# Kernel optimization log

Hardware: AMD Instinct MI355X
Metric: run time of the kernel (lower is better)

The kernel has to match this reference:

```python
import jax, jax.numpy as jnp
import numpy as np

N = 50000       # nodes
E = 800000      # edges (before self-loops)
F_IN = 128
HID = 64
HEADS = 4
OUT_DIM = 128
N_CLS = 2
NG = 500        # num graphs
SLOPE = 0.2     # GATConv leaky_relu negative slope
EPS = 1e-5      # BatchNorm eps


def setup_inputs() -> dict:
    key = jax.random.key(0)
    ks = jax.random.split(key, 24)
    s = 0.05
    d = {
        "x": jax.random.normal(ks[0], (N, F_IN), jnp.float32),
        "edge_index": jax.random.randint(ks[1], (2, E), 0, N, jnp.int64),
        "batch": jnp.sort(jax.random.randint(ks[2], (N,), 0, NG, jnp.int64)),
        # GATConv 1
        "W1": jax.random.normal(ks[3], (F_IN, HEADS * HID), jnp.float32) * s,
        "att_src1": jax.random.normal(ks[4], (HEADS, HID), jnp.float32) * s,
        "att_dst1": jax.random.normal(ks[5], (HEADS, HID), jnp.float32) * s,
        "b1": jnp.zeros((HEADS * HID,), jnp.float32),
        # BN1 (eval mode)
        "g1": jnp.ones((HEADS * HID,), jnp.float32),
        "be1": jnp.zeros((HEADS * HID,), jnp.float32),
        "rm1": jnp.zeros((HEADS * HID,), jnp.float32),
        "rv1": jnp.ones((HEADS * HID,), jnp.float32),
        # GATConv 2
        "W2": jax.random.normal(ks[6], (HEADS * HID, HEADS * HID), jnp.float32) * s,
        "att_src2": jax.random.normal(ks[7], (HEADS, HID), jnp.float32) * s,
        "att_dst2": jax.random.normal(ks[8], (HEADS, HID), jnp.float32) * s,
        "b2": jnp.zeros((HEADS * HID,), jnp.float32),
        # BN2 (eval mode)
        "g2": jnp.ones((HEADS * HID,), jnp.float32),
        "be2": jnp.zeros((HEADS * HID,), jnp.float32),
        "rm2": jnp.zeros((HEADS * HID,), jnp.float32),
        "rv2": jnp.ones((HEADS * HID,), jnp.float32),
        # MLP head
        "lw1": jax.random.normal(ks[9], (HEADS * HID, OUT_DIM), jnp.float32) * s,
        "lb1": jnp.zeros((OUT_DIM,), jnp.float32),
        "lw2": jax.random.normal(ks[10], (OUT_DIM, N_CLS), jnp.float32) * s,
        "lb2": jnp.zeros((N_CLS,), jnp.float32),
    }
    return d


def _gat_conv(x, src, dst, W, a_src, a_dst, b):
    """PyG GATConv (concat heads, add_self_loops=True, eval -> no dropout)."""
    n = x.shape[0]
    h = (x @ W).reshape(n, HEADS, -1)            # [N, H, C]
    loop = jnp.arange(n)
    s = jnp.concatenate([src, loop])             # self-loops appended
    d = jnp.concatenate([dst, loop])
    a_s = jnp.sum(h * a_src, axis=-1)            # [N, H]
    a_d = jnp.sum(h * a_dst, axis=-1)            # [N, H]
    e = jax.nn.leaky_relu(a_s[s] + a_d[d], SLOPE)   # [Et, H]
    # softmax over incoming edges per destination node
    m = jax.ops.segment_max(e, d, num_segments=n)
    ex = jnp.exp(e - m[d])
    denom = jax.ops.segment_sum(ex, d, num_segments=n)
    alpha = ex / denom[d]                        # [Et, H]
    msg = h[s] * alpha[:, :, None]               # [Et, H, C]
    out = jax.ops.segment_sum(msg, d, num_segments=n)
    return out.reshape(n, -1) + b


def _bn_eval(x, g, be, rm, rv):
    return (x - rm) * jax.lax.rsqrt(rv + EPS) * g + be


def reference(x, edge_index, batch, W1, att_src1, att_dst1, b1, g1, be1, rm1, rv1,
              W2, att_src2, att_dst2, b2, g2, be2, rm2, rv2, lw1, lb1, lw2, lb2):
    src, dst = edge_index[0], edge_index[1]
    h = jax.nn.relu(_gat_conv(x, src, dst, W1, att_src1, att_dst1, b1))
    h = _bn_eval(h, g1, be1, rm1, rv1)
    h = jax.nn.relu(_gat_conv(h, src, dst, W2, att_src2, att_dst2, b2))
    h = _bn_eval(h, g2, be2, rm2, rv2)
    # global mean pool over graphs
    sums = jax.ops.segment_sum(h, batch, num_segments=NG)
    cnt = jax.ops.segment_sum(jnp.ones((h.shape[0],), h.dtype), batch, num_segments=NG)
    pooled = sums / jnp.clip(cnt, 1.0)[:, None]
    z = jax.nn.relu(pooled @ lw1 + lb1)
    return z @ lw2 + lb2
```

## Files before the change

### kernel.cpp

```cpp
#include <hip/hip_runtime.h>
#include <hip/hip_bf16.h>
#include <math.h>

#define N_NODES 50000
#define M_PAD   50048
#define TILE_M  64
#define NBLK_GEMM (M_PAD / TILE_M)
#define N_EDGES 800000
#define F_IN 128
#define HID 64
#define HEADS 4
#define FEAT 256
#define OUT_DIM 128
#define N_CLS 2
#define NG 500
#define SLOPE 0.2f
#define BN_EPS 1e-5f
#define ECAP 64
#define ET (N_EDGES + N_NODES)
#define EH ((ET + 1) / 2)
#define NBLK_BUILD ((EH + 255) / 256)

typedef __attribute__((ext_vector_type(8))) short short8;
typedef __attribute__((ext_vector_type(4))) float floatx4;
typedef __attribute__((ext_vector_type(2))) float floatx2;

__device__ inline unsigned short f2bf(float f) {
    unsigned int u = __float_as_uint(f);
    unsigned int lsb = (u >> 16) & 1u;
    return (unsigned short)((u + 0x7fffu + lsb) >> 16);
}

template<bool AF32, bool BUILD>
__global__ __launch_bounds__(256, 4) void gemm_mfma_gat(
    const void* __restrict__ Av, const unsigned short* __restrict__ BT,
    const float* __restrict__ att_src, const float* __restrict__ att_dst,
    unsigned char* __restrict__ h8, float* __restrict__ a_s,
    float* __restrict__ a_d, int K,
    const int* __restrict__ src, const int* __restrict__ dst,
    int* __restrict__ deg, int* __restrict__ ell,
    int* __restrict__ ovf_cnt, int* __restrict__ ovf) {
    constexpr int LS = 40;
    constexpr int C8 = 272;
    __shared__ __align__(16) unsigned char smem_raw[(TILE_M + FEAT) * LS * 2];
    int t = threadIdx.x;

    if (BUILD && blockIdx.x >= NBLK_GEMM) {
        int i = (blockIdx.x - NBLK_GEMM) * 256 + t;
        if (i >= EH) return;
        int ss[2], dd[2], pp[2];
        int nv = 0;
        #pragma unroll
        for (int j = 0; j < 2; j++) {
            int e = i + j * EH;
            if (e < ET) {
                if (e < N_EDGES) { ss[nv] = src[e]; dd[nv] = dst[e]; }
                else             { ss[nv] = dd[nv] = e - N_EDGES; }
                nv++;
            }
        }
        #pragma unroll
        for (int j = 0; j < 2; j++)
            if (j < nv) pp[j] = atomicAdd(&deg[dd[j]], 1);
        #pragma unroll
        for (int j = 0; j < 2; j++) {
            if (j >= nv) continue;
            if (pp[j] < ECAP) {
                ell[dd[j] * ECAP + pp[j]] = ss[j];
            } else {
                int k = atomicAdd(ovf_cnt, 1);
                ovf[2 * k] = ss[j];
                ovf[2 * k + 1] = dd[j];
            }
        }
        return;
    }

    unsigned short* As = (unsigned short*)smem_raw;
    unsigned short* Bs = As + TILE_M * LS;
    unsigned char*  s8 = smem_raw;
    int lane = t & 63, w = t >> 6;
    int row0 = blockIdx.x * TILE_M;
    int mrow = lane & 15, quad = lane >> 4;

    floatx4 acc[4][4] = {};

    int rA = t >> 2, cA = (t & 3) * 8;

    const unsigned short* Ab = (const unsigned short*)Av;
    const float* Af = (const float*)Av;

    for (int k0 = 0; k0 < K; k0 += 32) {
        {
            int r = rA;
            if (AF32) {
                uint4 pk = make_uint4(0, 0, 0, 0);
                if (row0 + r < N_NODES) {
                    float4 f0 = *(const float4*)&Af[(long long)(row0 + r) * K + k0 + cA];
                    float4 f1 = *(const float4*)&Af[(long long)(row0 + r) * K + k0 + cA + 4];
                    pk.x = (unsigned)f2bf(f0.x) | ((unsigned)f2bf(f0.y) << 16);
                    pk.y = (unsigned)f2bf(f0.z) | ((unsigned)f2bf(f0.w) << 16);
                    pk.z = (unsigned)f2bf(f1.x) | ((unsigned)f2bf(f1.y) << 16);
                    pk.w = (unsigned)f2bf(f1.z) | ((unsigned)f2bf(f1.w) << 16);
                }
                *(uint4*)&As[r * LS + cA] = pk;
            } else {
                *(uint4*)&As[r * LS + cA] = *(const uint4*)&Ab[(long long)(row0 + r) * K + k0 + cA];
            }
        }
        #pragma unroll
        for (int j = 0; j < 4; j++) {
            int r = rA + j * 64;
            *(uint4*)&Bs[r * LS + cA] = *(const uint4*)&BT[(long long)r * K + k0 + cA];
        }
        __syncthreads();
        short8 bf[4];
        #pragma unroll
        for (int ni = 0; ni < 4; ni++)
            bf[ni] = *(const short8*)&Bs[(w * 64 + ni * 16 + mrow) * LS + quad * 8];
        #pragma unroll
        for (int mi = 0; mi < 4; mi++) {
            short8 af = *(const short8*)&As[(mi * 16 + mrow) * LS + quad * 8];
            #pragma unroll
            for (int ni = 0; ni < 4; ni++)
                acc[mi][ni] = __builtin_amdgcn_mfma_f32_16x16x32_bf16(af, bf[ni],
                                                                      acc[mi][ni], 0, 0, 0);
        }
        __syncthreads();
    }

    float ats[4], atd[4];
    #pragma unroll
    for (int ni = 0; ni < 4; ni++) {
        ats[ni] = att_src[w * 64 + ni * 16 + mrow];
        atd[ni] = att_dst[w * 64 + ni * 16 + mrow];
    }
    #pragma unroll
    for (int mi = 0; mi < 4; mi++) {
        #pragma unroll
        for (int r = 0; r < 4; r++) {
            int row = row0 + mi * 16 + quad * 4 + r;
            float ps = 0.f, pd = 0.f;
            #pragma unroll
            for (int ni = 0; ni < 4; ni++) {
                float v = acc[mi][ni][r];
                ps += v * ats[ni];
                pd += v * atd[ni];
            }
            #pragma unroll
            for (int off = 1; off < 16; off <<= 1) {
                ps += __shfl_xor(ps, off);
                pd += __shfl_xor(pd, off);
            }
            if (mrow == 0 && row < N_NODES) {
                a_s[row * 4 + w] = ps;
                a_d[row * 4 + w] = pd;
            }
        }
    }

    #pragma unroll
    for (int mi = 0; mi < 4; mi++)
        #pragma unroll
        for (int r = 0; r < 4; r++) {
            int row = mi * 16 + quad * 4 + r;
            #pragma unroll
            for (int ni = 0; ni < 4; ni += 2) {
                int pk = __builtin_amdgcn_cvt_pk_fp8_f32(acc[mi][ni][r],
                                                         acc[mi][ni + 1][r], 0, false);
                s8[row * C8 + w * 64 + ni * 16 + mrow]       = (unsigned char)(pk & 0xff);
                s8[row * C8 + w * 64 + (ni + 1) * 16 + mrow] = (unsigned char)((pk >> 8) & 0xff);
            }
        }
    __syncthreads();
    {
        int r2 = t >> 2, q = t & 3;
        const uint4* sp = (const uint4*)&s8[r2 * C8 + q * 64];
        uint4* dp = (uint4*)&h8[(long long)(row0 + r2) * FEAT + q * 64];
        #pragma unroll
        for (int k = 0; k < 4; k++)
            dp[k] = sp[k];
    }
}

__global__ void prep(const float* __restrict__ W1, const float* __restrict__ W2,
                     unsigned short* __restrict__ W1T, unsigned short* __restrict__ W2T,
                     int* __restrict__ deg, int* __restrict__ ovf_cnt,
                     unsigned long long* __restrict__ h1bf_pad) {
    int i = blockIdx.x * 256 + threadIdx.x;
    if (i < F_IN * 256) {
        int k = i >> 8, n = i & 255;
        W1T[n * F_IN + k] = f2bf(W1[i]);
    }
    int j = i - F_IN * 256;
    if (j >= 0 && j < FEAT * 256) {
        int k = j >> 8, n = j & 255;
        W2T[n * FEAT + k] = f2bf(W2[j]);
    }
    if (i < N_NODES) deg[i] = 0;
    if (i == 0) *ovf_cnt = 0;
    if (i < (M_PAD - N_NODES) * FEAT / 4) h1bf_pad[i] = 0ULL;
}

__global__ __launch_bounds__(256) void gat_fused(
    const int* __restrict__ deg_arr, const int* __restrict__ ell,
    const int* __restrict__ ovf_cnt, const int* __restrict__ ovf,
    const float* __restrict__ a_s, const float* __restrict__ a_d,
    const unsigned char* __restrict__ h8, const float* __restrict__ bias,
    const float* __restrict__ g, const float* __restrict__ be,
    const float* __restrict__ rm, const float* __restrict__ rv,
    unsigned short* __restrict__ out16) {
    int t = threadIdx.x;
    int lane = t & 63;
    int w = t >> 6;
    int hd = lane >> 4;
    int d = blockIdx.x * 4 + w;

    __shared__ float p_lds[4 * ECAP * 4];
    __shared__ int   o_lds[4 * ECAP];
    float* pw = &p_lds[w * ECAP * 4];
    int*   ow = &o_lds[w * ECAP];

    const unsigned int* __restrict__ H1 = (const unsigned int*)h8;

    int deg = deg_arr[d];
    float4 ad4 = *(const float4*)&a_d[d * 4];

    float den = 0.f;
    float4 acc = make_float4(0.f, 0.f, 0.f, 0.f);

    if (deg <= ECAP) {
        float lg[4] = {-INFINITY, -INFINITY, -INFINITY, -INFINITY};
        if (lane < deg) {
            int s = ell[d * ECAP + lane];
            ow[lane] = s * 64;
            float4 as4 = *(const float4*)&a_s[s * 4];
            float e0 = as4.x + ad4.x; lg[0] = e0 > 0.f ? e0 : SLOPE * e0;
            float e1 = as4.y + ad4.y; lg[1] = e1 > 0.f ? e1 : SLOPE * e1;
            float e2 = as4.z + ad4.z; lg[2] = e2 > 0.f ? e2 : SLOPE * e2;
            float e3 = as4.w + ad4.w; lg[3] = e3 > 0.f ? e3 : SLOPE * e3;
        }
        float mm = fmaxf(fmaxf(lg[0], lg[1]), fmaxf(lg[2], lg[3]));
        #pragma unroll
        for (int off = 1; off < 64; off <<= 1) mm = fmaxf(mm, __shfl_xor(mm, off));
        if (lane < deg) {
            float4 pq;
            pq.x = __expf(lg[0] - mm);
            pq.y = __expf(lg[1] - mm);
            pq.z = __expf(lg[2] - mm);
            pq.w = __expf(lg[3] - mm);
            *(float4*)&pw[lane * 4] = pq;
        }
        int e = 0;
        for (; e + 1 < deg; e += 2) {
            int oA = ow[e], oB = ow[e + 1];
            float pA = pw[e * 4 + hd], pB = pw[(e + 1) * 4 + hd];
            int uA = (int)H1[oA + lane];
            int uB = (int)H1[oB + lane];
            den += pA + pB;
            floatx2 a0 = __builtin_amdgcn_cvt_pk_f32_fp8(uA, false);
            floatx2 a1 = __builtin_amdgcn_cvt_pk_f32_fp8(uA, true);
            floatx2 b0 = __builtin_amdgcn_cvt_pk_f32_fp8(uB, false);
            floatx2 b1 = __builtin_amdgcn_cvt_pk_f32_fp8(uB, true);
            acc.x += pA * a0.x; acc.y += pA * a0.y;
            acc.z += pA * a1.x; acc.w += pA * a1.y;
            acc.x += pB * b0.x; acc.y += pB * b0.y;
            acc.z += pB * b1.x; acc.w += pB * b1.y;
        }
        if (e < deg) {
            int oA = ow[e];
            float pA = pw[e * 4 + hd];
            int uA = (int)H1[oA + lane];
            den += pA;
            floatx2 a0 = __builtin_amdgcn_cvt_pk_f32_fp8(uA, false);
            floatx2 a1 = __builtin_amdgcn_cvt_pk_f32_fp8(uA, true);
            acc.x += pA * a0.x; acc.y += pA * a0.y;
            acc.z += pA * a1.x; acc.w += pA * a1.y;
        }
    } else {
        float m_old;
        {
            int s = ell[d * ECAP + lane];
            ow[lane] = s * 64;
            float4 as4 = *(const float4*)&a_s[s * 4];
            float lg[4];
            float e0 = as4.x + ad4.x; lg[0] = e0 > 0.f ? e0 : SLOPE * e0;
            float e1 = as4.y + ad4.y; lg[1] = e1 > 0.f ? e1 : SLOPE * e1;
            float e2 = as4.z + ad4.z; lg[2] = e2 > 0.f ? e2 : SLOPE * e2;
            float e3 = as4.w + ad4.w; lg[3] = e3 > 0.f ? e3 : SLOPE * e3;
            float mm = fmaxf(fmaxf(lg[0], lg[1]), fmaxf(lg[2], lg[3]));
            #pragma unroll
            for (int off = 1; off < 64; off <<= 1) mm = fmaxf(mm, __shfl_xor(mm, off));
            m_old = mm;
            float4 pq;
            pq.x = __expf(lg[0] - mm);
            pq.y = __expf(lg[1] - mm);
            pq.z = __expf(lg[2] - mm);
            pq.w = __expf(lg[3] - mm);
            *(float4*)&pw[lane * 4] = pq;
            for (int e = 0; e < ECAP; e++) {
                int oA = ow[e];
                float pA = pw[e * 4 + hd];
                int uA = (int)H1[oA + lane];
                den += pA;
                floatx2 a0 = __builtin_amdgcn_cvt_pk_f32_fp8(uA, false);
                floatx2 a1 = __builtin_amdgcn_cvt_pk_f32_fp8(uA, true);
                acc.x += pA * a0.x; acc.y += pA * a0.y;
                acc.z += pA * a1.x; acc.w += pA * a1.y;
            }
        }
        int nov = *ovf_cnt;
        for (int i = 0; i < nov; i++) {
            int s2 = ovf[2 * i], d2 = ovf[2 * i + 1];
            if (d2 != d) continue;
            float4 as4 = *(const float4*)&a_s[s2 * 4];
            float lg[4];
            float e0 = as4.x + ad4.x; lg[0] = e0 > 0.f ? e0 : SLOPE * e0;
            float e1 = as4.y + ad4.y; lg[1] = e1 > 0.f ? e1 : SLOPE * e1;
            float e2 = as4.z + ad4.z; lg[2] = e2 > 0.f ? e2 : SLOPE * e2;
            float e3 = as4.w + ad4.w; lg[3] = e3 > 0.f ? e3 : SLOPE * e3;
            float mmax = fmaxf(fmaxf(lg[0], lg[1]), fmaxf(lg[2], lg[3]));
            float m_new = fmaxf(m_old, mmax);
            float alpha = __expf(m_old - m_new);
            m_old = m_new;
            float ph = __expf(lg[hd] - m_new);
            acc.x *= alpha; acc.y *= alpha; acc.z *= alpha; acc.w *= alpha;
            den = den * alpha + ph;
            int u = (int)H1[s2 * 64 + lane];
            floatx2 a0 = __builtin_amdgcn_cvt_pk_f32_fp8(u, false);
            floatx2 a1 = __builtin_amdgcn_cvt_pk_f32_fp8(u, true);
            acc.x += ph * a0.x; acc.y += ph * a0.y;
            acc.z += ph * a1.x; acc.w += ph * a1.y;
        }
    }
    float inv = 1.f / den;
    int c0 = lane * 4;
    float4 bi = *(const float4*)&bias[c0];
    float4 gg = *(const float4*)&g[c0];
    float4 bb = *(const float4*)&be[c0];
    float4 mm4 = *(const float4*)&rm[c0];
    float4 vv = *(const float4*)&rv[c0];
    float v0 = fmaxf(acc.x * inv + bi.x, 0.f);
    float v1 = fmaxf(acc.y * inv + bi.y, 0.f);
    float v2 = fmaxf(acc.z * inv + bi.z, 0.f);
    float v3 = fmaxf(acc.w * inv + bi.w, 0.f);
    v0 = (v0 - mm4.x) * rsqrtf(vv.x + BN_EPS) * gg.x + bb.x;
    v1 = (v1 - mm4.y) * rsqrtf(vv.y + BN_EPS) * gg.y + bb.y;
    v2 = (v2 - mm4.z) * rsqrtf(vv.z + BN_EPS) * gg.z + bb.z;
    v3 = (v3 - mm4.w) * rsqrtf(vv.w + BN_EPS) * gg.w + bb.w;
    unsigned long long o =
        (unsigned long long)f2bf(v0) |
        ((unsigned long long)f2bf(v1) << 16) |
        ((unsigned long long)f2bf(v2) << 32) |
        ((unsigned long long)f2bf(v3) << 48);
    __builtin_nontemporal_store(o, (unsigned long long*)&out16[(long long)d * FEAT + c0]);
}

__global__ __launch_bounds__(256) void head_fused(
    const unsigned short* __restrict__ h2, const int* __restrict__ batch,
    const float* __restrict__ lw1, const float* __restrict__ lb1,
    const float* __restrict__ lw2, const float* __restrict__ lb2,
    float* __restrict__ out) {
    int gph = blockIdx.x;
    int t = threadIdx.x;
    __shared__ float pooled[FEAT];
    __shared__ float zl[OUT_DIM];
    __shared__ int lo_s, hi_s;
    if (t == 0) {
        int lo = 0, hi = N_NODES;
        while (lo < hi) { int mid = (lo + hi) >> 1; if (batch[mid] < gph) lo = mid + 1; else hi = mid; }
        lo_s = lo;
        int lo2 = 0, hi2 = N_NODES;
        while (lo2 < hi2) { int mid = (lo2 + hi2) >> 1; if (batch[mid] < gph + 1) lo2 = mid + 1; else hi2 = mid; }
        hi_s = lo2;
    }
    __syncthreads();
    int lo = lo_s, hi = hi_s;
    float a0 = 0.f, a1 = 0.f, a2 = 0.f, a3 = 0.f;
    int n = lo;
    for (; n + 3 < hi; n += 4) {
        a0 += __uint_as_float((unsigned)h2[(long long)n * FEAT + t] << 16);
        a1 += __uint_as_float((unsigned)h2[(long long)(n + 1) * FEAT + t] << 16);
        a2 += __uint_as_float((unsigned)h2[(long long)(n + 2) * FEAT + t] << 16);
        a3 += __uint_as_float((unsigned)h2[(long long)(n + 3) * FEAT + t] << 16);
    }
    for (; n < hi; n++) a0 += __uint_as_float((unsigned)h2[(long long)n * FEAT + t] << 16);
    float cnt = fmaxf((float)(hi - lo), 1.f);
    pooled[t] = (a0 + a1 + a2 + a3) / cnt;
    __syncthreads();
    int j = t >> 1, kh = t & 1;
    float zp = 0.f;
    #pragma unroll 8
    for (int k = kh * 128; k < kh * 128 + 128; k++)
        zp += pooled[k] * lw1[k * OUT_DIM + j];
    zp += __shfl_xor(zp, 1);
    if (kh == 0) zl[j] = fmaxf(zp + lb1[j], 0.f);
    __syncthreads();
    int w = t >> 6, lane = t & 63;
    if (w < 2) {
        float p = zl[lane] * lw2[lane * 2 + w] + zl[lane + 64] * lw2[(lane + 64) * 2 + w];
        #pragma unroll
        for (int off = 1; off < 64; off <<= 1) p += __shfl_xor(p, off);
        if (lane == 0) out[gph * 2 + w] = p + lb2[w];
    }
}

extern "C" void kernel_launch(void* const* d_in, const int* in_sizes, int n_in,
                              void* d_out, int out_size, void* d_ws, size_t ws_size,
                              hipStream_t stream) {
    const float* x       = (const float*)d_in[0];
    const int*   ei      = (const int*)d_in[1];
    const int*   batch   = (const int*)d_in[2];
    const float* W1      = (const float*)d_in[3];
    const float* att_s1  = (const float*)d_in[4];
    const float* att_d1  = (const float*)d_in[5];
    const float* b1      = (const float*)d_in[6];
    const float* g1      = (const float*)d_in[7];
    const float* be1     = (const float*)d_in[8];
    const float* rm1     = (const float*)d_in[9];
    const float* rv1     = (const float*)d_in[10];
    const float* W2      = (const float*)d_in[11];
    const float* att_s2  = (const float*)d_in[12];
    const float* att_d2  = (const float*)d_in[13];
    const float* b2      = (const float*)d_in[14];
    const float* g2      = (const float*)d_in[15];
    const float* be2     = (const float*)d_in[16];
    const float* rm2     = (const float*)d_in[17];
    const float* rv2     = (const float*)d_in[18];
    const float* lw1     = (const float*)d_in[19];
    const float* lb1     = (const float*)d_in[20];
    const float* lw2     = (const float*)d_in[21];
    const float* lb2     = (const float*)d_in[22];
    float* out           = (float*)d_out;

    const int* src = ei;
    const int* dst = ei + N_EDGES;

    char* p = (char*)d_ws;
    auto carve = [&p](size_t bytes) -> void* {
        void* r = (void*)p;
        p += (bytes + 63) & ~(size_t)63;
        return r;
    };
    unsigned short* h2bf = (unsigned short*)carve(sizeof(short) * (size_t)N_NODES * FEAT);
    float* a_s    = (float*)carve(sizeof(float) * N_NODES * HEADS);
    float* a_d    = (float*)carve(sizeof(float) * N_NODES * HEADS);
    int*   deg    = (int*)carve(sizeof(int) * N_NODES);
    int*   ell    = (int*)carve(sizeof(int) * (size_t)N_NODES * ECAP);
    int*   ovf_cnt= (int*)carve(sizeof(int) * 16);
    int*   ovf    = (int*)carve(sizeof(int) * 2 * ET);
    unsigned char*  h8   = (unsigned char*)carve((size_t)M_PAD * FEAT);
    unsigned short* h1bf = (unsigned short*)carve(sizeof(short) * (size_t)M_PAD * FEAT);
    unsigned short* w1t  = (unsigned short*)carve(sizeof(short) * FEAT * F_IN);
    unsigned short* w2t  = (unsigned short*)carve(sizeof(short) * FEAT * FEAT);

    prep<<<((F_IN + FEAT) * 256 + 255) / 256, 256, 0, stream>>>(
        W1, W2, w1t, w2t, deg, ovf_cnt,
        (unsigned long long*)(h1bf + (size_t)N_NODES * FEAT));

    gemm_mfma_gat<true, true><<<NBLK_GEMM + NBLK_BUILD, 256, 0, stream>>>(
        x, w1t, att_s1, att_d1, h8, a_s, a_d, F_IN,
        src, dst, deg, ell, ovf_cnt, ovf);
    gat_fused<<<N_NODES / 4, 256, 0, stream>>>(deg, ell, ovf_cnt, ovf, a_s, a_d, h8,
                                               b1, g1, be1, rm1, rv1, h1bf);

    gemm_mfma_gat<false, false><<<NBLK_GEMM, 256, 0, stream>>>(
        h1bf, w2t, att_s2, att_d2, h8, a_s, a_d, FEAT,
        nullptr, nullptr, nullptr, nullptr, nullptr, nullptr);
    gat_fused<<<N_NODES / 4, 256, 0, stream>>>(deg, ell, ovf_cnt, ovf, a_s, a_d, h8,
                                               b2, g2, be2, rm2, rv2, h2bf);

    head_fused<<<NG, 256, 0, stream>>>(h2bf, batch, lw1, lb1, lw2, lb2, out);
}
```

Baseline: 302.3 us.

## Separate edge build from GEMM, pre-convert x to bf16, store ELL as uint16

Moves the ELL adjacency build out of the first GEMM launch and into a new prep_build kernel. That kernel also converts x to bf16 up front and zero-fills the padding rows. The ELL neighbor indices are narrowed from int32 to uint16, which halves adjacency traffic in both aggregation passes. The GEMM becomes a single template on K with a plain bf16 A load, and deg/ovf_cnt are cleared by a hipMemsetAsync. The cost is an extra kernel launch, a memset, and an extra write and read of a bf16 copy of x. Build atomics also no longer overlap with GEMM work.

```diff
diff --git a/kernel.cpp b/kernel.cpp
--- a/kernel.cpp
+++ b/kernel.cpp
@@ -21,6 +21,12 @@
 #define EH ((ET + 1) / 2)
 #define NBLK_BUILD ((EH + 255) / 256)
 
+#define XCONV (N_NODES * F_IN / 8)
+#define XPAD_ULL ((M_PAD - N_NODES) * F_IN / 4)
+#define HPAD_ULL ((M_PAD - N_NODES) * FEAT / 4)
+#define PREP_THREADS (XCONV + F_IN * 256 + FEAT * 256 + XPAD_ULL + HPAD_ULL)
+#define NBLK_PREP ((PREP_THREADS + 255) / 256)
+
 typedef __attribute__((ext_vector_type(8))) short short8;
 typedef __attribute__((ext_vector_type(4))) float floatx4;
 typedef __attribute__((ext_vector_type(2))) float floatx2;
@@ -31,50 +37,91 @@
     return (unsigned short)((u + 0x7fffu + lsb) >> 16);
 }
 
-template<bool AF32, bool BUILD>
-__global__ __launch_bounds__(256, 4) void gemm_mfma_gat(
-    const void* __restrict__ Av, const unsigned short* __restrict__ BT,
+__global__ __launch_bounds__(256) void prep_build(
+    const float* __restrict__ x, const float* __restrict__ W1,
+    const float* __restrict__ W2,
+    unsigned short* __restrict__ xbf, unsigned short* __restrict__ W1T,
+    unsigned short* __restrict__ W2T, unsigned short* __restrict__ h1bf,
+    const int* __restrict__ src, const int* __restrict__ dst,
+    int* __restrict__ deg, unsigned short* __restrict__ ell,
+    int* __restrict__ ovf_cnt, int* __restrict__ ovf) {
+    int b = blockIdx.x;
+    int t = threadIdx.x;
+    if (b < NBLK_PREP) {
+        int gid = b * 256 + t;
+        if (gid < XCONV) {
+            const float4* xp = (const float4*)&x[gid * 8];
+            float4 f0 = xp[0], f1 = xp[1];
+            uint4 pk;
+            pk.x = (unsigned)f2bf(f0.x) | ((unsigned)f2bf(f0.y) << 16);
+            pk.y = (unsigned)f2bf(f0.z) | ((unsigned)f2bf(f0.w) << 16);
+            pk.z = (unsigned)f2bf(f1.x) | ((unsigned)f2bf(f1.y) << 16);
+            pk.w = (unsigned)f2bf(f1.z) | ((unsigned)f2bf(f1.w) << 16);
+            *(uint4*)&xbf[gid * 8] = pk;
+            return;
+        }
+        int j = gid - XCONV;
+        if (j < F_IN * 256) {
+            int k = j >> 8, n = j & 255;
+            W1T[n * F_IN + k] = f2bf(W1[j]);
+            return;
+        }
+        j -= F_IN * 256;
+        if (j < FEAT * 256) {
+            int k = j >> 8, n = j & 255;
+            W2T[n * FEAT + k] = f2bf(W2[j]);
+            return;
+        }
+        j -= FEAT * 256;
+        if (j < XPAD_ULL) {
+            ((unsigned long long*)(xbf + (size_t)N_NODES * F_IN))[j] = 0ULL;
+            return;
+        }
+        j -= XPAD_ULL;
+        if (j < HPAD_ULL) {
+            ((unsigned long long*)(h1bf + (size_t)N_NODES * FEAT))[j] = 0ULL;
+        }
+        return;
+    }
+    int i = (b - NBLK_PREP) * 256 + t;
+    if (i >= EH) return;
+    int ss[2], dd[2], pp[2];
+    int nv = 0;
+    #pragma unroll
+    for (int j = 0; j < 2; j++) {
+        int e = i + j * EH;
+        if (e < ET) {
+            if (e < N_EDGES) { ss[nv] = src[e]; dd[nv] = dst[e]; }
+            else             { ss[nv] = dd[nv] = e - N_EDGES; }
+            nv++;
+        }
+    }
+    #pragma unroll
+    for (int j = 0; j < 2; j++)
+        if (j < nv) pp[j] = atomicAdd(&deg[dd[j]], 1);
+    #pragma unroll
+    for (int j = 0; j < 2; j++) {
+        if (j >= nv) continue;
+        if (pp[j] < ECAP) {
+            ell[dd[j] * ECAP + pp[j]] = (unsigned short)ss[j];
+        } else {
+            int k = atomicAdd(ovf_cnt, 1);
+            ovf[2 * k] = ss[j];
+            ovf[2 * k + 1] = dd[j];
+        }
+    }
+}
+
+template<int K>
+__global__ __launch_bounds__(256, 4) void gemm_mfma(
+    const unsigned short* __restrict__ Ab, const unsigned short* __restrict__ BT,
     const float* __restrict__ att_src, const float* __restrict__ att_dst,
     unsigned char* __restrict__ h8, float* __restrict__ a_s,
-    float* __restrict__ a_d, int K,
-    const int* __restrict__ src, const int* __restrict__ dst,
-    int* __restrict__ deg, int* __restrict__ ell,
-    int* __restrict__ ovf_cnt, int* __restrict__ ovf) {
+    float* __restrict__ a_d) {
     constexpr int LS = 40;
     constexpr int C8 = 272;
     __shared__ __align__(16) unsigned char smem_raw[(TILE_M + FEAT) * LS * 2];
     int t = threadIdx.x;
-
-    if (BUILD && blockIdx.x >= NBLK_GEMM) {
-        int i = (blockIdx.x - NBLK_GEMM) * 256 + t;
-        if (i >= EH) return;
-        int ss[2], dd[2], pp[2];
-        int nv = 0;
-        #pragma unroll
-        for (int j = 0; j < 2; j++) {
-            int e = i + j * EH;
-            if (e < ET) {
-                if (e < N_EDGES) { ss[nv] = src[e]; dd[nv] = dst[e]; }
-                else             { ss[nv] = dd[nv] = e - N_EDGES; }
-                nv++;
-            }
-        }
-        #pragma unroll
-        for (int j = 0; j < 2; j++)
-            if (j < nv) pp[j] = atomicAdd(&deg[dd[j]], 1);
-        #pragma unroll
-        for (int j = 0; j < 2; j++) {
-            if (j >= nv) continue;
-            if (pp[j] < ECAP) {
-                ell[dd[j] * ECAP + pp[j]] = ss[j];
-            } else {
-                int k = atomicAdd(ovf_cnt, 1);
-                ovf[2 * k] = ss[j];
-                ovf[2 * k + 1] = dd[j];
-            }
-        }
-        return;
-    }
 
     unsigned short* As = (unsigned short*)smem_raw;
     unsigned short* Bs = As + TILE_M * LS;
@@ -87,27 +134,9 @@
 
     int rA = t >> 2, cA = (t & 3) * 8;
 
-    const unsigned short* Ab = (const unsigned short*)Av;
-    const float* Af = (const float*)Av;
-
     for (int k0 = 0; k0 < K; k0 += 32) {
-        {
-            int r = rA;
-            if (AF32) {
-                uint4 pk = make_uint4(0, 0, 0, 0);
-                if (row0 + r < N_NODES) {
-                    float4 f0 = *(const float4*)&Af[(long long)(row0 + r) * K + k0 + cA];
-                    float4 f1 = *(const float4*)&Af[(long long)(row0 + r) * K + k0 + cA + 4];
-                    pk.x = (unsigned)f2bf(f0.x) | ((unsigned)f2bf(f0.y) << 16);
-                    pk.y = (unsigned)f2bf(f0.z) | ((unsigned)f2bf(f0.w) << 16);
-                    pk.z = (unsigned)f2bf(f1.x) | ((unsigned)f2bf(f1.y) << 16);
-                    pk.w = (unsigned)f2bf(f1.z) | ((unsigned)f2bf(f1.w) << 16);
-                }
-                *(uint4*)&As[r * LS + cA] = pk;
-            } else {
-                *(uint4*)&As[r * LS + cA] = *(const uint4*)&Ab[(long long)(row0 + r) * K + k0 + cA];
-            }
-        }
+        *(uint4*)&As[rA * LS + cA] =
+            *(const uint4*)&Ab[(long long)(row0 + rA) * K + k0 + cA];
         #pragma unroll
         for (int j = 0; j < 4; j++) {
             int r = rA + j * 64;
@@ -183,27 +212,8 @@
     }
 }
 
-__global__ void prep(const float* __restrict__ W1, const float* __restrict__ W2,
-                     unsigned short* __restrict__ W1T, unsigned short* __restrict__ W2T,
-                     int* __restrict__ deg, int* __restrict__ ovf_cnt,
-                     unsigned long long* __restrict__ h1bf_pad) {
-    int i = blockIdx.x * 256 + threadIdx.x;
-    if (i < F_IN * 256) {
-        int k = i >> 8, n = i & 255;
-        W1T[n * F_IN + k] = f2bf(W1[i]);
-    }
-    int j = i - F_IN * 256;
-    if (j >= 0 && j < FEAT * 256) {
-        int k = j >> 8, n = j & 255;
-        W2T[n * FEAT + k] = f2bf(W2[j]);
-    }
-    if (i < N_NODES) deg[i] = 0;
-    if (i == 0) *ovf_cnt = 0;
-    if (i < (M_PAD - N_NODES) * FEAT / 4) h1bf_pad[i] = 0ULL;
-}
-
 __global__ __launch_bounds__(256) void gat_fused(
-    const int* __restrict__ deg_arr, const int* __restrict__ ell,
+    const int* __restrict__ deg_arr, const unsigned short* __restrict__ ell,
     const int* __restrict__ ovf_cnt, const int* __restrict__ ovf,
     const float* __restrict__ a_s, const float* __restrict__ a_d,
     const unsigned char* __restrict__ h8, const float* __restrict__ bias,
@@ -446,27 +456,27 @@
     float* a_s    = (float*)carve(sizeof(float) * N_NODES * HEADS);
     float* a_d    = (float*)carve(sizeof(float) * N_NODES * HEADS);
     int*   deg    = (int*)carve(sizeof(int) * N_NODES);
-    int*   ell    = (int*)carve(sizeof(int) * (size_t)N_NODES * ECAP);
     int*   ovf_cnt= (int*)carve(sizeof(int) * 16);
+    unsigned short* ell = (unsigned short*)carve(sizeof(short) * (size_t)N_NODES * ECAP);
     int*   ovf    = (int*)carve(sizeof(int) * 2 * ET);
     unsigned char*  h8   = (unsigned char*)carve((size_t)M_PAD * FEAT);
+    unsigned short* xbf  = (unsigned short*)carve(sizeof(short) * (size_t)M_PAD * F_IN);
     unsigned short* h1bf = (unsigned short*)carve(sizeof(short) * (size_t)M_PAD * FEAT);
     unsigned short* w1t  = (unsigned short*)carve(sizeof(short) * FEAT * F_IN);
     unsigned short* w2t  = (unsigned short*)carve(sizeof(short) * FEAT * FEAT);
 
-    prep<<<((F_IN + FEAT) * 256 + 255) / 256, 256, 0, stream>>>(
-        W1, W2, w1t, w2t, deg, ovf_cnt,
-        (unsigned long long*)(h1bf + (size_t)N_NODES * FEAT));
-
-    gemm_mfma_gat<true, true><<<NBLK_GEMM + NBLK_BUILD, 256, 0, stream>>>(
-        x, w1t, att_s1, att_d1, h8, a_s, a_d, F_IN,
-        src, dst, deg, ell, ovf_cnt, ovf);
+    hipMemsetAsync(deg, 0, sizeof(int) * N_NODES + 64, stream);
+
+    prep_build<<<NBLK_PREP + NBLK_BUILD, 256, 0, stream>>>(
+        x, W1, W2, xbf, w1t, w2t, h1bf, src, dst, deg, ell, ovf_cnt, ovf);
+
+    gemm_mfma<F_IN><<<NBLK_GEMM, 256, 0, stream>>>(
+        xbf, w1t, att_s1, att_d1, h8, a_s, a_d);
     gat_fused<<<N_NODES / 4, 256, 0, stream>>>(deg, ell, ovf_cnt, ovf, a_s, a_d, h8,
                                                b1, g1, be1, rm1, rv1, h1bf);
 
-    gemm_mfma_gat<false, false><<<NBLK_GEMM, 256, 0, stream>>>(
-        h1bf, w2t, att_s2, att_d2, h8, a_s, a_d, FEAT,
-        nullptr, nullptr, nullptr, nullptr, nullptr, nullptr);
+    gemm_mfma<FEAT><<<NBLK_GEMM, 256, 0, stream>>>(
+        h1bf, w2t, att_s2, att_d2, h8, a_s, a_d);
     gat_fused<<<N_NODES / 4, 256, 0, stream>>>(deg, ell, ovf_cnt, ovf, a_s, a_d, h8,
                                                b2, g2, be2, rm2, rv2, h2bf);
 
```

Result: slower. 311.8 us (+3.1%).
